# Kernel optimization log

Measured on AMD Instinct MI355X. Metric: run time of the kernel, lower is better.

## Reference

```python
import jax, jax.numpy as jnp
import numpy as np

N_WIRES = 10
N_BLOCKS = 4
DIM = 2 ** N_WIRES


def _tables(n):
    # Basis-state bit tables. Wire 0 is the most-significant bit (torchquantum convention).
    s = np.arange(2 ** n)
    bits = (s[None, :] >> (n - 1 - np.arange(n))[:, None]) & 1  # [n, 2^n]
    zval = (1 - 2 * bits).astype(np.float32)  # PauliZ eigenvalue per wire per basis state
    # Composition of the circular CNOT ring (0,1),(1,2),...,(n-2,n-1),(n-1,0)
    # as a single basis permutation: state'[s] = state[P[s]].
    pairs = [(i, i + 1) for i in range(n - 1)] + [(n - 1, 0)]
    P = s.copy()
    for c, t in pairs:
        bit = (s >> (n - 1 - c)) & 1
        g = s ^ (bit << (n - 1 - t))  # CNOT maps new[s] = old[g(s)]
        P = P[g]
    return zval, P


_ZVAL_NP, _PERM_NP = _tables(N_WIRES)


def setup_inputs() -> dict:
    key = jax.random.key(0)
    k1, k2 = jax.random.split(key)
    x = jax.random.normal(k1, (2048, N_WIRES), jnp.float32)
    params = jax.random.normal(k2, (N_BLOCKS, 6, N_WIRES), jnp.float32)
    return {"x": x, "params": params}


def _rz_all(state, theta, zval):
    # RZ(theta_w) on every wire fused into one diagonal phase over the full statevector.
    # RZ = diag(e^{-i t/2}, e^{+i t/2}); exponent sign = -zval (bit0 -> -1).
    phase = jnp.exp((-0.5j) * (theta @ zval).astype(jnp.complex64))  # [2^n]
    return state * phase[None, :]


def _ry_all(state, theta, bsz):
    # RY(theta_w) on each wire w: 2x2 rotation applied along that wire's axis.
    for w in range(N_WIRES):
        left = 2 ** w
        right = DIM // (2 * left)
        s4 = state.reshape(bsz, left, 2, right)
        c = jnp.cos(theta[w] * 0.5)
        s_ = jnp.sin(theta[w] * 0.5)
        U = jnp.stack([jnp.stack([c, -s_]), jnp.stack([s_, c])]).astype(jnp.complex64)
        s4 = jnp.einsum('bixk,jx->bijk', s4, U)
        state = s4.reshape(bsz, DIM)
    return state


def reference(x, params):
    zval = jnp.asarray(_ZVAL_NP)
    perm = jnp.asarray(_PERM_NP)
    bsz = x.shape[0]
    state = jnp.zeros((bsz, DIM), jnp.complex64).at[:, 0].set(1.0)  # |0...0>
    for k in range(N_BLOCKS):
        p = params[k]
        # NOTE: the original module's "rx" layers are constructed with tq.RZ,
        # so each block is RZ, RY, RZ, CNOT-ring, RZ, RY, RZ, CNOT-ring.
        state = _rz_all(state, p[0], zval)
        state = _ry_all(state, p[1], bsz)
        state = _rz_all(state, p[2], zval)
        state = state[:, perm]
        state = _rz_all(state, p[3], zval)
        state = _ry_all(state, p[4], bsz)
        state = _rz_all(state, p[5], zval)
        state = state[:, perm]
        if k != N_BLOCKS - 1:
            # data re-uploading encoder: RZ(x[:, w]) on wire w, batch-dependent diagonal
            enc = jnp.exp((-0.5j) * (x @ zval).astype(jnp.complex64))  # [B, 2^n]
            state = state * enc
    probs = state.real ** 2 + state.imag ** 2  # [B, 2^n]
    out = probs @ zval.T  # MeasureAll PauliZ -> [B, n_wires]
    return out[None]  # [1, B, n_wires]
```

## Files before the change

kernel.cpp:

```cpp
#include <hip/hip_runtime.h>

#define NW 10

typedef float v2f __attribute__((ext_vector_type(2)));

template<int CTRL>
__device__ __forceinline__ float fdpp(float v) {
    return __int_as_float(__builtin_amdgcn_mov_dpp(__float_as_int(v), CTRL, 0xF, 0xF, true));
}
template<int PAT>
__device__ __forceinline__ float fswz(float v) {
    return __int_as_float(__builtin_amdgcn_ds_swizzle(__float_as_int(v), PAT));
}
__device__ __forceinline__ float fbperm(int addr, float v) {
    return __int_as_float(__builtin_amdgcn_ds_bpermute(addr, __float_as_int(v)));
}

__global__ void precompute_kernel(const float* __restrict__ params, float2* __restrict__ tab) {
    const int j = blockIdx.x * 256 + threadIdx.x;
    if (j < 7 * 1024) {
        const int d = j >> 10, jj = j & 1023;
        const int W = jj >> 8, lane = jj & 63, r = (jj >> 6) & 3;
        const int s = (W << 8) | (lane << 2) | r;
        const int q = s ^ (s >> 1) ^ ((s & 1) * 0x300);
        const float* thA;
        const float* thB;
        if (d < 4) {
            thA = params + (d * 6 + 3) * NW;
            thB = params + (d * 6 + 2) * NW;
        } else {
            const int k = d - 4;
            thA = params + ((k + 1) * 6 + 0) * NW;
            thB = params + (k * 6 + 5) * NW;
        }
        float ang = 0.f;
#pragma unroll
        for (int w = 0; w < NW; ++w) {
            ang += thA[w] * (((s >> (9 - w)) & 1) ? 0.5f : -0.5f);
            ang += thB[w] * (((q >> (9 - w)) & 1) ? 0.5f : -0.5f);
        }
        float sn, cs;
        __sincosf(ang, &sn, &cs);
        tab[j] = make_float2(cs, sn);
    } else if (j < 7 * 1024 + 80) {
        const int i = j - 7 * 1024;
        const int ry = i / NW, w = i % NW;
        const int k = ry >> 1, ii = ry & 1;
        const float* th = params + (k * 6 + (ii ? 4 : 1)) * NW;
        float sn, cs;
        __sincosf(0.5f * th[w], &sn, &cs);
        tab[7 * 1024 + i] = make_float2(cs, sn);
    }
}


#define DPP_STAGE(CTRL, CW, BIT) do {                                          \
    const float2 cw_ = (CW);                                                   \
    const float ss_ = (lane & (BIT)) ? cw_.y : -cw_.y;                         \
    _Pragma("unroll")                                                          \
    for (int u_ = 0; u_ < 16; ++u_) {                                          \
        v2f p_;                                                                \
        p_.x = fdpp<CTRL>(st[u_].x);                                           \
        p_.y = fdpp<CTRL>(st[u_].y);                                           \
        st[u_] = cw_.x * st[u_] + ss_ * p_;                                    \
    }                                                                          \
} while (0)

#define SWZ_STAGE(PAT, CW, BIT) do {                                           \
    const float2 cw_ = (CW);                                                   \
    const float ss_ = (lane & (BIT)) ? cw_.y : -cw_.y;                         \
    v2f p_[16];                                                                \
    _Pragma("unroll")                                                          \
    for (int u_ = 0; u_ < 16; ++u_) {                                          \
        p_[u_].x = fswz<PAT>(st[u_].x);                                        \
        p_[u_].y = fswz<PAT>(st[u_].y);                                        \
    }                                                                          \
    _Pragma("unroll")                                                          \
    for (int u_ = 0; u_ < 16; ++u_) st[u_] = cw_.x * st[u_] + ss_ * p_[u_];    \
} while (0)

#define X32_STAGE(CW) do {                                                     \
    const float2 cw_ = (CW);                                                   \
    const float ss_ = (lane & 32) ? cw_.y : -cw_.y;                            \
    v2f p_[16];                                                                \
    _Pragma("unroll")                                                          \
    for (int u_ = 0; u_ < 16; ++u_) {                                          \
        p_[u_].x = __shfl_xor(st[u_].x, 32, 64);                               \
        p_[u_].y = __shfl_xor(st[u_].y, 32, 64);                               \
    }                                                                          \
    _Pragma("unroll")                                                          \
    for (int u_ = 0; u_ < 16; ++u_) st[u_] = cw_.x * st[u_] + ss_ * p_[u_];    \
} while (0)

__global__ __launch_bounds__(256, 2) void qsim_kernel(const float* __restrict__ x,
                                                      const float2* __restrict__ tab,
                                                      float* __restrict__ out) {
    const int t    = threadIdx.x;
    const int W    = t >> 6;
    const int lane = t & 63;
    const int b    = blockIdx.x * 4 + W;
    const float2* ry_tab = tab + 7 * 1024;

    const int l0 = lane & 1, l1 = (lane >> 1) & 1, l2 = (lane >> 2) & 1,
              l3 = (lane >> 3) & 1, l4 = (lane >> 4) & 1, l5 = (lane >> 5) & 1;

    const int lp = (l0 ^ l1) | ((l1 ^ l2) << 1) | ((l2 ^ l3) << 2)
                 | ((l3 ^ l4) << 3) | ((l4 ^ l5) << 4) | (l5 << 5);
    const int pa0 = lp << 2;
    const int pa1 = pa0 ^ 128;
    const int par = l0 ^ l1 ^ l2 ^ l3 ^ l4 ^ l5;

    v2f st[16];
    float2 xp[16];
    float2 tq[16];

    {
        const float* xb = x + b * NW;
        float xv[NW];
#pragma unroll
        for (int w = 0; w < NW; ++w) xv[w] = xb[w];
        float A = 0.f;
#pragma unroll
        for (int w = 0; w < NW; ++w) A += xv[w];
        float hb = -0.5f * A;
        if (l0) hb += xv[7];
        if (l1) hb += xv[6];
        if (l2) hb += xv[5];
        if (l3) hb += xv[4];
        if (l4) hb += xv[3];
        if (l5) hb += xv[2];
#pragma unroll
        for (int u = 0; u < 16; ++u) {
            float ang = hb;
            if (u & 1) ang += xv[9];
            if (u & 2) ang += xv[8];
            if (u & 4) ang += xv[1];
            if (u & 8) ang += xv[0];
            float sn, cs;
            __sincosf(ang, &sn, &cs);
            xp[u] = make_float2(cs, sn);
        }
    }

    auto pre = [&](int d) {
        const float2* tb = tab + (d << 10) + lane;
#pragma unroll
        for (int u = 0; u < 16; ++u)
            tq[u] = tb[((u & 3) << 6) | ((u >> 2) << 8)];
    };

    auto initC = [&]() {
        const float2 r9 = ry_tab[9], r8 = ry_tab[8], r7 = ry_tab[7], r6 = ry_tab[6],
                     r5 = ry_tab[5], r4 = ry_tab[4], r3 = ry_tab[3], r2 = ry_tab[2],
                     r1 = ry_tab[1], r0 = ry_tab[0];
        float P6 = (l0 ? r7.y : r7.x) * (l1 ? r6.y : r6.x) * (l2 ? r5.y : r5.x)
                 * (l3 ? r4.y : r4.x) * (l4 ? r3.y : r3.x) * (l5 ? r2.y : r2.x);
#pragma unroll
        for (int u = 0; u < 16; ++u) {
            float v = P6 * ((u & 1) ? r9.y : r9.x) * ((u & 2) ? r8.y : r8.x)
                         * ((u & 4) ? r1.y : r1.x) * ((u & 8) ? r0.y : r0.x);
            st[u] = (v2f){v, 0.f};
        }
    };

    auto bflyL = [&](float2 cw, int m) {
#pragma unroll
        for (int u = 0; u < 16; ++u)
            if (!(u & m)) {
                const int v = u | m;
                const v2f a = st[u];
                st[u] = cw.x * a - cw.y * st[v];
                st[v] = cw.y * a + cw.x * st[v];
            }
    };

    auto ry = [&](int ridx) {
        const float2* rt = ry_tab + ridx * NW;
        bflyL(rt[9], 1);
        bflyL(rt[8], 2);
        bflyL(rt[1], 4);
        bflyL(rt[0], 8);
        DPP_STAGE(0xB1, rt[7], 1);
        DPP_STAGE(0x4E, rt[6], 2);
        SWZ_STAGE(0x101F, rt[5], 4);
        DPP_STAGE(0x128, rt[4], 8);
        SWZ_STAGE(0x401F, rt[3], 16);
        X32_STAGE(rt[2]);
    };

    auto permApply = [&](int mode) {
        v2f ns[16];
#pragma unroll
        for (int u = 0; u < 16; ++u) {
            const int u0 = u & 1, u1 = (u >> 1) & 1, u2 = (u >> 2) & 1, u3 = (u >> 3) & 1;
            const int a = (u0 ^ u1) | (u1 << 1) | ((u0 ^ u2 ^ u3) << 2) | ((u0 ^ u3) << 3);
            const v2f v = (par ^ u2) ? st[a ^ 2] : st[a];
            const int ad = u2 ? pa1 : pa0;
            ns[u].x = fbperm(ad, v.x);
            ns[u].y = fbperm(ad, v.y);
        }
#pragma unroll
        for (int u = 0; u < 16; ++u) {
            float cx = tq[u].x, cy = tq[u].y;
            if (mode) {
                const float tx = cx, ty = cy;
                cx = tx * xp[u].x - ty * xp[u].y;
                cy = tx * xp[u].y + ty * xp[u].x;
            }
            st[u] = (v2f){cx * ns[u].x - cy * ns[u].y,
                          cy * ns[u].x + cx * ns[u].y};
        }
    };

#pragma unroll 1
    for (int k = 0; k < 4; ++k) {
        pre(k);
        if (k == 0) initC();
        else        ry(2 * k);
        permApply(0);
        if (k < 3) pre(4 + k);
        ry(2 * k + 1);
        if (k < 3) permApply(1);
    }

    float pr[16];
#pragma unroll
    for (int u = 0; u < 16; ++u) pr[u] = st[u].x * st[u].x + st[u].y * st[u].y;

    float q0[4], q1[4], q2[4];
#pragma unroll
    for (int g = 0; g < 4; ++g) {
        const float a = pr[4 * g] + pr[4 * g + 1], bb = pr[4 * g + 2] + pr[4 * g + 3];
        const float c = pr[4 * g] - pr[4 * g + 1], d = pr[4 * g + 2] - pr[4 * g + 3];
        q0[g] = a + bb;
        q1[g] = a - bb;
        q2[g] = c - d;
    }
    const float R23   = q0[0] - q0[1] - q0[2] + q0[3];
    const float R123  = q1[0] - q1[1] - q1[2] + q1[3];
    const float R0123 = q2[0] - q2[1] - q2[2] + q2[3];
    const float R012  = q2[0] - q2[1] + q2[2] - q2[3];

    const int P5 = l5, P4 = l4 ^ P5, P3 = l3 ^ P4, P2 = l2 ^ P3, P1 = l1 ^ P2, P0 = l0 ^ P1;

    float acc[NW];
    acc[0] = P0 ? -R012 : R012;
    acc[1] = R23;
    acc[2] = P5 ? -R23 : R23;
    acc[3] = P4 ? -R23 : R23;
    acc[4] = P3 ? -R23 : R23;
    acc[5] = P2 ? -R23 : R23;
    acc[6] = P1 ? -R23 : R23;
    acc[7] = P0 ? -R23 : R23;
    acc[8] = P0 ? -R123 : R123;
    acc[9] = P0 ? -R0123 : R0123;

#pragma unroll
    for (int w = 0; w < NW; ++w) {
        float a = acc[w];
        a += fdpp<0xB1>(a);
        a += fdpp<0x4E>(a);
        a += fswz<0x101F>(a);
        a += fdpp<0x128>(a);
        a += fswz<0x401F>(a);
        a += __shfl_xor(a, 32, 64);
        acc[w] = a;
    }
    if (lane == 0) {
        float2* o = (float2*)(out + b * NW);
        o[0] = make_float2(acc[0], acc[1]);
        o[1] = make_float2(acc[2], acc[3]);
        o[2] = make_float2(acc[4], acc[5]);
        o[3] = make_float2(acc[6], acc[7]);
        o[4] = make_float2(acc[8], acc[9]);
    }
}

extern "C" void kernel_launch(void* const* d_in, const int* in_sizes, int n_in,
                              void* d_out, int out_size, void* d_ws, size_t ws_size,
                              hipStream_t stream) {
    const float* x      = (const float*)d_in[0];
    const float* params = (const float*)d_in[1];
    float* out          = (float*)d_out;
    float2* tab         = (float2*)d_ws;
    (void)in_sizes; (void)n_in; (void)out_size; (void)ws_size;
    precompute_kernel<<<29, 256, 0, stream>>>(params, tab);
    qsim_kernel<<<512, 256, 0, stream>>>(x, tab, out);
}
```

Before: 81.08 us.

## Split each statevector across two wavefronts with LDS exchange for permutation

Each batch sample is now simulated by two wavefronts that each hold half the statevector (8 amplitudes per lane instead of 16), with wire 0 split across the waves. The CNOT-ring permutation moves from ds_bpermute into a shared-memory exchange that is double-buffered, and the wire-0 RY rotation is fused into that exchange. This halves the register pressure per thread and doubles the wave count, aiming for more occupancy and latency hiding. In exchange it adds __syncthreads barriers, LDS traffic, and a cross-wave reduction at the end.

New measurement: 79.29 us. 2.2% less time.

```diff
diff --git a/kernel.cpp b/kernel.cpp
--- a/kernel.cpp
+++ b/kernel.cpp
@@ -11,17 +11,14 @@
 template<int PAT>
 __device__ __forceinline__ float fswz(float v) {
     return __int_as_float(__builtin_amdgcn_ds_swizzle(__float_as_int(v), PAT));
-}
-__device__ __forceinline__ float fbperm(int addr, float v) {
-    return __int_as_float(__builtin_amdgcn_ds_bpermute(addr, __float_as_int(v)));
 }
 
 __global__ void precompute_kernel(const float* __restrict__ params, float2* __restrict__ tab) {
     const int j = blockIdx.x * 256 + threadIdx.x;
     if (j < 7 * 1024) {
         const int d = j >> 10, jj = j & 1023;
-        const int W = jj >> 8, lane = jj & 63, r = (jj >> 6) & 3;
-        const int s = (W << 8) | (lane << 2) | r;
+        const int Wj = jj >> 8, lane = jj & 63, r = (jj >> 6) & 3;
+        const int s = (Wj << 8) | (lane << 2) | r;
         const int q = s ^ (s >> 1) ^ ((s & 1) * 0x300);
         const float* thA;
         const float* thB;
@@ -58,7 +55,7 @@
     const float2 cw_ = (CW);                                                   \
     const float ss_ = (lane & (BIT)) ? cw_.y : -cw_.y;                         \
     _Pragma("unroll")                                                          \
-    for (int u_ = 0; u_ < 16; ++u_) {                                          \
+    for (int u_ = 0; u_ < 8; ++u_) {                                           \
         v2f p_;                                                                \
         p_.x = fdpp<CTRL>(st[u_].x);                                           \
         p_.y = fdpp<CTRL>(st[u_].y);                                           \
@@ -69,50 +66,53 @@
 #define SWZ_STAGE(PAT, CW, BIT) do {                                           \
     const float2 cw_ = (CW);                                                   \
     const float ss_ = (lane & (BIT)) ? cw_.y : -cw_.y;                         \
-    v2f p_[16];                                                                \
-    _Pragma("unroll")                                                          \
-    for (int u_ = 0; u_ < 16; ++u_) {                                          \
+    v2f p_[8];                                                                 \
+    _Pragma("unroll")                                                          \
+    for (int u_ = 0; u_ < 8; ++u_) {                                           \
         p_[u_].x = fswz<PAT>(st[u_].x);                                        \
         p_[u_].y = fswz<PAT>(st[u_].y);                                        \
     }                                                                          \
     _Pragma("unroll")                                                          \
-    for (int u_ = 0; u_ < 16; ++u_) st[u_] = cw_.x * st[u_] + ss_ * p_[u_];    \
+    for (int u_ = 0; u_ < 8; ++u_) st[u_] = cw_.x * st[u_] + ss_ * p_[u_];     \
 } while (0)
 
 #define X32_STAGE(CW) do {                                                     \
     const float2 cw_ = (CW);                                                   \
     const float ss_ = (lane & 32) ? cw_.y : -cw_.y;                            \
-    v2f p_[16];                                                                \
-    _Pragma("unroll")                                                          \
-    for (int u_ = 0; u_ < 16; ++u_) {                                          \
+    v2f p_[8];                                                                 \
+    _Pragma("unroll")                                                          \
+    for (int u_ = 0; u_ < 8; ++u_) {                                           \
         p_[u_].x = __shfl_xor(st[u_].x, 32, 64);                               \
         p_[u_].y = __shfl_xor(st[u_].y, 32, 64);                               \
     }                                                                          \
     _Pragma("unroll")                                                          \
-    for (int u_ = 0; u_ < 16; ++u_) st[u_] = cw_.x * st[u_] + ss_ * p_[u_];    \
+    for (int u_ = 0; u_ < 8; ++u_) st[u_] = cw_.x * st[u_] + ss_ * p_[u_];     \
 } while (0)
 
-__global__ __launch_bounds__(256, 2) void qsim_kernel(const float* __restrict__ x,
+__global__ __launch_bounds__(128, 4) void qsim_kernel(const float* __restrict__ x,
                                                       const float2* __restrict__ tab,
                                                       float* __restrict__ out) {
+    __shared__ v2f ex[2][1024];
+    __shared__ float sred[2][NW];
+
     const int t    = threadIdx.x;
     const int W    = t >> 6;
     const int lane = t & 63;
-    const int b    = blockIdx.x * 4 + W;
+    const int b    = blockIdx.x;
     const float2* ry_tab = tab + 7 * 1024;
 
     const int l0 = lane & 1, l1 = (lane >> 1) & 1, l2 = (lane >> 2) & 1,
               l3 = (lane >> 3) & 1, l4 = (lane >> 4) & 1, l5 = (lane >> 5) & 1;
 
-    const int lp = (l0 ^ l1) | ((l1 ^ l2) << 1) | ((l2 ^ l3) << 2)
-                 | ((l3 ^ l4) << 3) | ((l4 ^ l5) << 4) | (l5 << 5);
-    const int pa0 = lp << 2;
-    const int pa1 = pa0 ^ 128;
-    const int par = l0 ^ l1 ^ l2 ^ l3 ^ l4 ^ l5;
-
-    v2f st[16];
-    float2 xp[16];
-    float2 tq[16];
+    const int base = (l0 ^ l1) | ((l1 ^ l2) << 1) | ((l2 ^ l3) << 2)
+                   | ((l3 ^ l4) << 3) | ((l4 ^ l5) << 4) | (l5 << 5)
+                   | (l0 << 7) | (W << 8) | (W << 9);
+    const int widx = lane | (W << 9);
+
+    v2f st[8];
+    float2 xp[8];
+    float2 tq[8];
+    int bs = 0;
 
     {
         const float* xb = x + b * NW;
@@ -129,13 +129,13 @@
         if (l3) hb += xv[4];
         if (l4) hb += xv[3];
         if (l5) hb += xv[2];
-#pragma unroll
-        for (int u = 0; u < 16; ++u) {
+        if (W)  hb += xv[0];
+#pragma unroll
+        for (int u = 0; u < 8; ++u) {
             float ang = hb;
             if (u & 1) ang += xv[9];
             if (u & 2) ang += xv[8];
             if (u & 4) ang += xv[1];
-            if (u & 8) ang += xv[0];
             float sn, cs;
             __sincosf(ang, &sn, &cs);
             xp[u] = make_float2(cs, sn);
@@ -143,10 +143,10 @@
     }
 
     auto pre = [&](int d) {
-        const float2* tb = tab + (d << 10) + lane;
-#pragma unroll
-        for (int u = 0; u < 16; ++u)
-            tq[u] = tb[((u & 3) << 6) | ((u >> 2) << 8)];
+        const float2* tb = tab + (d << 10) + lane + (W << 9);
+#pragma unroll
+        for (int u = 0; u < 8; ++u)
+            tq[u] = tb[((u & 3) << 6) | (((u >> 2) & 1) << 8)];
     };
 
     auto initC = [&]() {
@@ -155,17 +155,18 @@
                      r1 = ry_tab[1], r0 = ry_tab[0];
         float P6 = (l0 ? r7.y : r7.x) * (l1 ? r6.y : r6.x) * (l2 ? r5.y : r5.x)
                  * (l3 ? r4.y : r4.x) * (l4 ? r3.y : r3.x) * (l5 ? r2.y : r2.x);
-#pragma unroll
-        for (int u = 0; u < 16; ++u) {
+        P6 *= (W ? r0.y : r0.x);
+#pragma unroll
+        for (int u = 0; u < 8; ++u) {
             float v = P6 * ((u & 1) ? r9.y : r9.x) * ((u & 2) ? r8.y : r8.x)
-                         * ((u & 4) ? r1.y : r1.x) * ((u & 8) ? r0.y : r0.x);
+                         * ((u & 4) ? r1.y : r1.x);
             st[u] = (v2f){v, 0.f};
         }
     };
 
     auto bflyL = [&](float2 cw, int m) {
 #pragma unroll
-        for (int u = 0; u < 16; ++u)
+        for (int u = 0; u < 8; ++u)
             if (!(u & m)) {
                 const int v = u | m;
                 const v2f a = st[u];
@@ -179,7 +180,6 @@
         bflyL(rt[9], 1);
         bflyL(rt[8], 2);
         bflyL(rt[1], 4);
-        bflyL(rt[0], 8);
         DPP_STAGE(0xB1, rt[7], 1);
         DPP_STAGE(0x4E, rt[6], 2);
         SWZ_STAGE(0x101F, rt[5], 4);
@@ -188,19 +188,28 @@
         X32_STAGE(rt[2]);
     };
 
-    auto permApply = [&](int mode) {
-        v2f ns[16];
-#pragma unroll
-        for (int u = 0; u < 16; ++u) {
-            const int u0 = u & 1, u1 = (u >> 1) & 1, u2 = (u >> 2) & 1, u3 = (u >> 3) & 1;
-            const int a = (u0 ^ u1) | (u1 << 1) | ((u0 ^ u2 ^ u3) << 2) | ((u0 ^ u3) << 3);
-            const v2f v = (par ^ u2) ? st[a ^ 2] : st[a];
-            const int ad = u2 ? pa1 : pa0;
-            ns[u].x = fbperm(ad, v.x);
-            ns[u].y = fbperm(ad, v.y);
-        }
-#pragma unroll
-        for (int u = 0; u < 16; ++u) {
+    auto permFuse = [&](int mode, float2 cw0, bool withB) {
+        v2f* B = ex[bs]; bs ^= 1;
+#pragma unroll
+        for (int u = 0; u < 8; ++u) B[widx + (u << 6)] = st[u];
+        __syncthreads();
+        const float sb = W ? cw0.y : -cw0.y;
+        constexpr int msk[8] = {0x000, 0x340, 0x0C0, 0x380, 0x120, 0x260, 0x1E0, 0x2A0};
+        v2f ns[8];
+#pragma unroll
+        for (int u = 0; u < 8; ++u) {
+            const int si = base ^ msk[u];
+            const v2f a = B[si];
+            if (withB) {
+                const v2f p = B[si ^ 0x200];
+                const float sw = (u & 1) ? -sb : sb;
+                ns[u] = cw0.x * a + sw * p;
+            } else {
+                ns[u] = a;
+            }
+        }
+#pragma unroll
+        for (int u = 0; u < 8; ++u) {
             float cx = tq[u].x, cy = tq[u].y;
             if (mode) {
                 const float tx = cx, ty = cy;
@@ -212,34 +221,52 @@
         }
     };
 
+    auto w0x = [&](float2 cw0) {
+        v2f* B = ex[bs]; bs ^= 1;
+#pragma unroll
+        for (int u = 0; u < 8; ++u) B[widx + (u << 6)] = st[u];
+        __syncthreads();
+        const float sw = W ? cw0.y : -cw0.y;
+#pragma unroll
+        for (int u = 0; u < 8; ++u) {
+            const v2f p = B[(widx ^ 0x200) + (u << 6)];
+            st[u] = cw0.x * st[u] + sw * p;
+        }
+    };
+
 #pragma unroll 1
     for (int k = 0; k < 4; ++k) {
         pre(k);
         if (k == 0) initC();
         else        ry(2 * k);
-        permApply(0);
+        permFuse(0, ry_tab[(2 * k) * NW], k != 0);
         if (k < 3) pre(4 + k);
         ry(2 * k + 1);
-        if (k < 3) permApply(1);
-    }
-
-    float pr[16];
-#pragma unroll
-    for (int u = 0; u < 16; ++u) pr[u] = st[u].x * st[u].x + st[u].y * st[u].y;
-
-    float q0[4], q1[4], q2[4];
-#pragma unroll
-    for (int g = 0; g < 4; ++g) {
+        if (k < 3) permFuse(1, ry_tab[(2 * k + 1) * NW], true);
+        else       w0x(ry_tab[7 * NW]);
+    }
+
+    float pr[8];
+#pragma unroll
+    for (int u = 0; u < 8; ++u) pr[u] = st[u].x * st[u].x + st[u].y * st[u].y;
+
+    float q0[2], q1[2], q2[2];
+#pragma unroll
+    for (int g = 0; g < 2; ++g) {
         const float a = pr[4 * g] + pr[4 * g + 1], bb = pr[4 * g + 2] + pr[4 * g + 3];
         const float c = pr[4 * g] - pr[4 * g + 1], d = pr[4 * g + 2] - pr[4 * g + 3];
         q0[g] = a + bb;
         q1[g] = a - bb;
         q2[g] = c - d;
     }
-    const float R23   = q0[0] - q0[1] - q0[2] + q0[3];
-    const float R123  = q1[0] - q1[1] - q1[2] + q1[3];
-    const float R0123 = q2[0] - q2[1] - q2[2] + q2[3];
-    const float R012  = q2[0] - q2[1] + q2[2] - q2[3];
+    const float S0 = q0[0] - q0[1];
+    const float S1 = q1[0] - q1[1];
+    const float S2 = q2[0] - q2[1];
+    const float sg = W ? -1.f : 1.f;
+    const float R23   = sg * S0;
+    const float R123  = sg * S1;
+    const float R0123 = sg * S2;
+    const float R012  = S2;
 
     const int P5 = l5, P4 = l4 ^ P5, P3 = l3 ^ P4, P2 = l2 ^ P3, P1 = l1 ^ P2, P0 = l0 ^ P1;
 
@@ -267,13 +294,11 @@
         acc[w] = a;
     }
     if (lane == 0) {
-        float2* o = (float2*)(out + b * NW);
-        o[0] = make_float2(acc[0], acc[1]);
-        o[1] = make_float2(acc[2], acc[3]);
-        o[2] = make_float2(acc[4], acc[5]);
-        o[3] = make_float2(acc[6], acc[7]);
-        o[4] = make_float2(acc[8], acc[9]);
-    }
+#pragma unroll
+        for (int w = 0; w < NW; ++w) sred[W][w] = acc[w];
+    }
+    __syncthreads();
+    if (t < NW) out[b * NW + t] = sred[0][t] + sred[1][t];
 }
 
 extern "C" void kernel_launch(void* const* d_in, const int* in_sizes, int n_in,
@@ -285,5 +310,5 @@
     float2* tab         = (float2*)d_ws;
     (void)in_sizes; (void)n_in; (void)out_size; (void)ws_size;
     precompute_kernel<<<29, 256, 0, stream>>>(params, tab);
-    qsim_kernel<<<512, 256, 0, stream>>>(x, tab, out);
-}
+    qsim_kernel<<<2048, 128, 0, stream>>>(x, tab, out);
+}
```
